# Kernel optimization log

Measured on AMD Instinct MI355X. Metric: run time of the kernel, lower is better.

Reference implementation:

```python
import jax, jax.numpy as jnp
import numpy as np

B, C, H, W = 2, 256, 64, 64  # C = in_channels; x has 2*C channels
DQ = C // 16


def setup_inputs() -> dict:
    key = jax.random.key(0)
    ks = jax.random.split(key, 10)
    s = 0.05
    return {
        "x": jax.random.normal(ks[0], (B, 2 * C, H, W), dtype=jnp.float32),
        "Wq": jax.random.normal(ks[1], (DQ, C), dtype=jnp.float32) * s,
        "bq": jax.random.normal(ks[2], (DQ,), dtype=jnp.float32) * s,
        "Wk": jax.random.normal(ks[3], (DQ, C), dtype=jnp.float32) * s,
        "bk": jax.random.normal(ks[4], (DQ,), dtype=jnp.float32) * s,
        "Wv": jax.random.normal(ks[5], (C, C), dtype=jnp.float32) * s,
        "bv": jax.random.normal(ks[6], (C,), dtype=jnp.float32) * s,
        "Wpt": jax.random.normal(ks[7], (C, 2 * C), dtype=jnp.float32) * s,
        "bpt": jax.random.normal(ks[8], (C,), dtype=jnp.float32) * s,
        "gamma": jnp.full((1,), 0.5, dtype=jnp.float32),  # original inits to 0; nonzero for a non-trivial output
    }


def _conv1x1(x, Wt, b):
    # 1x1 conv == per-pixel linear map over channels
    return jnp.einsum("bchw,dc->bdhw", x, Wt) + b[None, :, None, None]


def reference(x, Wq, bq, Wk, bk, Wv, bv, Wpt, bpt, gamma):
    n = x.shape[1] // 2
    x1, x2 = x[:, :n], x[:, n:]
    b, c, h, w = x1.shape
    hw = h * w

    def qkv(xi):
        q = _conv1x1(xi, Wq, bq).reshape(b, DQ, hw)   # [B,dq,HW]
        k = _conv1x1(xi, Wk, bk).reshape(b, DQ, hw)   # [B,dq,HW]
        v = _conv1x1(xi, Wv, bv).reshape(b, c, hw)    # [B,C,HW]
        return q, k, v

    q1, k1, v1 = qkv(x1)
    q2, k2, v2 = qkv(x2)

    # attn[b,i,j] = softmax_j( q[:,i] . k[:,j] )  (no scaling, as in original)
    attn1 = jax.nn.softmax(jnp.einsum("bdi,bdj->bij", q1, k1), axis=-1)  # [B,HW,HW]
    attn2 = jax.nn.softmax(jnp.einsum("bdi,bdj->bij", q2, k2), axis=-1)

    def apply_attn(v, attn):
        # out[b,c,i] = sum_j v[b,c,j] * attn[b,i,j]
        return jnp.einsum("bcj,bij->bci", v, attn).reshape(b, c, h, w)

    out11 = apply_attn(v1, attn1)
    out12 = apply_attn(v2, attn1)
    out21 = apply_attn(v1, attn2)
    out22 = apply_attn(v2, attn2)

    o1 = _conv1x1(jnp.concatenate([out11, out12], axis=1), Wpt, bpt)  # [B,C,H,W]
    o2 = _conv1x1(jnp.concatenate([out21, out22], axis=1), Wpt, bpt)

    out = gamma * jnp.concatenate([o1, o2], axis=1) + x
    return out
```

## Files before the change

kernel.cpp:

```cpp
#include <hip/hip_runtime.h>
#include <hip/hip_bf16.h>


#define HW 4096
#define CC 256
#define DQ 16

typedef __hip_bfloat16 bf16;
struct alignas(8) bh4 { bf16 x, y, z, w; };
typedef __bf16 bf16x8 __attribute__((ext_vector_type(8)));
typedef float  f32x4  __attribute__((ext_vector_type(4)));

static __device__ __forceinline__ float b2f(bf16 v) { return __bfloat162float(v); }
static __device__ __forceinline__ float ldf(const void* p, size_t i, bool isb) {
    return isb ? b2f(((const bf16*)p)[i]) : ((const float*)p)[i];
}

static __device__ __forceinline__ void load_lds16(const void* g, void* l) {
    __builtin_amdgcn_global_load_lds(
        (const __attribute__((address_space(1))) unsigned int*)g,
        (__attribute__((address_space(3))) unsigned int*)l, 16, 0, 0);
}

static __device__ __forceinline__ bf16x8 ones8() {
    union { unsigned int u[4]; bf16x8 v; } t;
    t.u[0] = t.u[1] = t.u[2] = t.u[3] = 0x3F803F80u;
    return t.v;
}

__global__ void __launch_bounds__(256)
prep_xt(const void* __restrict__ xsrc,
        const void* __restrict__ Wq_r, const void* __restrict__ bq_r,
        const void* __restrict__ Wk_r, const void* __restrict__ bk_r,
        const void* __restrict__ Wv_r, const void* __restrict__ bv_r,
        const void* __restrict__ Wpt_r, const void* __restrict__ bpt_r,
        const void* __restrict__ gam_r,
        float* __restrict__ bqf, float* __restrict__ bkf, float* __restrict__ gamf,
        bf16* __restrict__ Wqb, bf16* __restrict__ Wkb,
        bf16* __restrict__ McB, float* __restrict__ btot, bf16* __restrict__ Xt,
        const unsigned short* __restrict__ probe) {
    __shared__ float T[64][65];
    int bx = blockIdx.x, tid = threadIdx.x;
    bool isb = probe[0] != 0;
    if (bx < 512) {
        int d = bx >> 1;
        int c = ((bx & 1) << 8) + tid;
        int half = c >> 8, cm = c & 255;
        float acc = 0.f;
        for (int e = 0; e < 256; ++e)
            acc = fmaf(ldf(Wpt_r, (size_t)d * 512 + half * 256 + e, isb),
                       ldf(Wv_r, (size_t)e * 256 + cm, isb), acc);
        McB[d * 512 + c] = __float2bfloat16(acc);
    } else if (bx == 512) {
        int d = tid;
        float acc = ldf(bpt_r, d, isb);
        for (int e = 0; e < 256; ++e)
            acc = fmaf(ldf(Wpt_r, (size_t)d * 512 + e, isb) +
                       ldf(Wpt_r, (size_t)d * 512 + 256 + e, isb),
                       ldf(bv_r, e, isb), acc);
        btot[d] = acc;
    } else if (bx < 545) {
        int id = bx - 513;
        const void* s = id < 16 ? Wq_r : Wk_r;
        bf16* dst = id < 16 ? Wqb : Wkb;
        int i = (id & 15) * 256 + tid;
        dst[i] = __float2bfloat16(ldf(s, i, isb));
    } else if (bx == 545) {
        if (tid < 16) bqf[tid] = ldf(bq_r, tid, isb);
        else if (tid < 32) bkf[tid - 16] = ldf(bk_r, tid - 16, isb);
        else if (tid == 32) gamf[0] = ldf(gam_r, 0, isb);
    } else {
        int id = bx - 546;
        int j0 = (id & 63) * 64, e0 = ((id >> 6) & 7) * 64, b = id >> 9;
        int j_l = tid & 63, er0 = (tid >> 6) * 16;
#pragma unroll
        for (int r = 0; r < 16; ++r) {
            size_t src = ((size_t)(b * 512 + e0 + er0 + r)) * HW + j0 + j_l;
            T[er0 + r][j_l] = ldf(xsrc, src, isb);
        }
        __syncthreads();
        int e_w = tid & 63, jr0 = (tid >> 6) * 16;
#pragma unroll
        for (int r = 0; r < 16; ++r)
            Xt[((size_t)b * HW + j0 + jr0 + r) * 512 + e0 + e_w] =
                __float2bfloat16(T[e_w][jr0 + r]);
    }
}

__global__ void __launch_bounds__(256, 2)
qku(const bf16* __restrict__ Xt,
    const bf16* __restrict__ Wqb, const float* __restrict__ bqf,
    const bf16* __restrict__ Wkb, const float* __restrict__ bkf,
    bf16* __restrict__ Qb, bf16* __restrict__ Kb,
    const bf16* __restrict__ McB, bf16* __restrict__ Ub) {
    __shared__ __align__(16) bf16 sA[64 * 64];
    __shared__ __align__(16) bf16 sB[128 * 64];
    int tid = threadIdx.x;
    int lane = tid & 63, wave = tid >> 6;
    int ln = lane & 15, q = lane >> 4;
    int bx = blockIdx.x;

    if (bx < 256) {
        int bh = bx >> 6;
        int b = bh >> 1, h = bh & 1;
        int j0 = (bx & 63) * 64 + wave * 16;
        bf16x8 aQ[8], aK[8];
#pragma unroll
        for (int kk = 0; kk < 8; ++kk) {
            aQ[kk] = *(const bf16x8*)&Wqb[ln * 256 + kk * 32 + q * 8];
            aK[kk] = *(const bf16x8*)&Wkb[ln * 256 + kk * 32 + q * 8];
        }
        const bf16* Xrow = Xt + ((size_t)b * HW + j0 + ln) * 512 + h * 256;
        f32x4 dQ = {0.f, 0.f, 0.f, 0.f}, dK = {0.f, 0.f, 0.f, 0.f};
#pragma unroll
        for (int kk = 0; kk < 8; ++kk) {
            bf16x8 bxv = *(const bf16x8*)&Xrow[kk * 32 + q * 8];
            dQ = __builtin_amdgcn_mfma_f32_16x16x32_bf16(aQ[kk], bxv, dQ, 0, 0, 0);
            dK = __builtin_amdgcn_mfma_f32_16x16x32_bf16(aK[kk], bxv, dK, 0, 0, 0);
        }
        size_t rowoff = ((size_t)bh * HW + j0 + ln) * 32;
        bh4 oq, ok;
        oq.x = __float2bfloat16(dQ[0] + bqf[q * 4 + 0]);
        oq.y = __float2bfloat16(dQ[1] + bqf[q * 4 + 1]);
        oq.z = __float2bfloat16(dQ[2] + bqf[q * 4 + 2]);
        oq.w = __float2bfloat16(dQ[3] + bqf[q * 4 + 3]);
        ok.x = __float2bfloat16(dK[0] + bkf[q * 4 + 0]);
        ok.y = __float2bfloat16(dK[1] + bkf[q * 4 + 1]);
        ok.z = __float2bfloat16(dK[2] + bkf[q * 4 + 2]);
        ok.w = __float2bfloat16(dK[3] + bkf[q * 4 + 3]);
        bh4 z; z.x = z.y = z.z = z.w = __float2bfloat16(0.f);
        *(bh4*)&Qb[rowoff + q * 4] = oq;
        *(bh4*)&Qb[rowoff + 16 + q * 4] = z;
        *(bh4*)&Kb[rowoff + q * 4] = ok;
        *(bh4*)&Kb[rowoff + 16 + q * 4] = z;
        return;
    }

    int id = bx - 256;
    int wm = (wave >> 1) * 32, wn = (wave & 1) * 64;
    int j0 = (id & 31) * 128, c0 = ((id >> 5) & 3) * 64, b = id >> 7;
    const bf16* Xb = Xt + (size_t)b * HW * 512;
    f32x4 acc[2][4];
#pragma unroll
    for (int mi = 0; mi < 2; ++mi)
#pragma unroll
        for (int ni = 0; ni < 4; ++ni)
#pragma unroll
            for (int r = 0; r < 4; ++r) acc[mi][ni][r] = 0.f;

    for (int e0 = 0; e0 < 512; e0 += 64) {
        __syncthreads();
#pragma unroll
        for (int r = 0; r < 2; ++r) {
            int s = r * 256 + tid;
            int row = s >> 3, jc = s & 7, jg = jc ^ (row & 7);
            load_lds16(McB + (size_t)(c0 + row) * 512 + e0 + jg * 8, sA + s * 8);
        }
#pragma unroll
        for (int r = 0; r < 4; ++r) {
            int s = r * 256 + tid;
            int row = s >> 3, jc = s & 7, jg = jc ^ (row & 7);
            load_lds16(Xb + (size_t)(j0 + row) * 512 + e0 + jg * 8, sB + s * 8);
        }
        __syncthreads();
#pragma unroll
        for (int kh = 0; kh < 2; ++kh) {
            bf16x8 af[2], bfv[4];
#pragma unroll
            for (int mi = 0; mi < 2; ++mi) {
                int row = wm + mi * 16 + ln;
                int jc = (kh * 4 + q) ^ (row & 7);
                af[mi] = *(const bf16x8*)&sA[row * 64 + jc * 8];
            }
#pragma unroll
            for (int ni = 0; ni < 4; ++ni) {
                int row = wn + ni * 16 + ln;
                int jc = (kh * 4 + q) ^ (row & 7);
                bfv[ni] = *(const bf16x8*)&sB[row * 64 + jc * 8];
            }
#pragma unroll
            for (int mi = 0; mi < 2; ++mi)
#pragma unroll
                for (int ni = 0; ni < 4; ++ni)
                    acc[mi][ni] = __builtin_amdgcn_mfma_f32_16x16x32_bf16(
                        af[mi], bfv[ni], acc[mi][ni], 0, 0, 0);
        }
    }
#pragma unroll
    for (int mi = 0; mi < 2; ++mi)
#pragma unroll
        for (int r = 0; r < 4; ++r) {
            int c = c0 + wm + mi * 16 + q * 4 + r;
#pragma unroll
            for (int ni = 0; ni < 4; ++ni) {
                int j = j0 + wn + ni * 16 + ln;
                Ub[((size_t)(b * CC + c)) * HW + j] = __float2bfloat16(acc[mi][ni][r]);
            }
        }
}

__global__ void __launch_bounds__(256, 2)
flash_attn(const bf16* __restrict__ Ub, const bf16* __restrict__ Qb,
           const bf16* __restrict__ Kb, const float* __restrict__ btot,
           const void* __restrict__ xorig, const float* __restrict__ gamf,
           void* __restrict__ outv, const unsigned short* __restrict__ probe) {
    __shared__ __align__(16) bf16 sU[2][128 * 64];
    __shared__ __align__(16) bf16 sK[2][4 * 64 * 8];
    __shared__ __align__(16) bf16 sE[64 * 64];
    int tid  = threadIdx.x;
    int lane = tid & 63, wave = tid >> 6;
    int ln = lane & 15, q = lane >> 4;
    int wm = (wave & 1) * 64, wn = (wave >> 1) * 32;

    int bid = blockIdx.x;
    int panel = bid & 7;
    int i0 = (bid >> 3) * 64;
    int c0 = (panel & 1) * 128;
    int bh = panel >> 1;
    int b = bh >> 1, h = bh & 1;

    const bf16* Ubb = Ub + (size_t)b * CC * HW + (size_t)c0 * HW;
    const bf16* Kbh = Kb + (size_t)bh * HW * 32;
    const bf16x8 ONE = ones8();

    bf16x8 bq = *(const bf16x8*)&Qb[((size_t)bh * HW + i0 + wave * 16 + ln) * 32 + q * 8];

    f32x4 acc[4][2], accS[2];
#pragma unroll
    for (int ni = 0; ni < 2; ++ni) {
#pragma unroll
        for (int r = 0; r < 4; ++r) accS[ni][r] = 0.f;
#pragma unroll
        for (int mi = 0; mi < 4; ++mi)
#pragma unroll
            for (int r = 0; r < 4; ++r) acc[mi][ni][r] = 0.f;
    }

    int i_loc = wave * 16 + ln;
    int wchunk0 = (q >> 1);
    int woff = (q & 1) * 4;

    auto stage_u = [&](int tn, int bufn) {
#pragma unroll
        for (int r = 0; r < 4; ++r) {
            int s = r * 256 + tid;
            int row = s >> 3, jc = s & 7, jg = jc ^ (row & 7);
            load_lds16(Ubb + (size_t)row * HW + tn * 64 + jg * 8, &sU[bufn][s * 8]);
        }
    };
    auto stage_k = [&](int tn, int bufn) {
        load_lds16(Kbh + ((size_t)(tn * 64 + (tid >> 6) * 16 + (tid & 15))) * 32
                       + ((tid >> 4) & 3) * 8,
                   &sK[bufn][tid * 8]);
    };

    stage_u(0, 0);
    stage_k(0, 0);
    asm volatile("s_waitcnt vmcnt(0)" ::: "memory");
    __builtin_amdgcn_sched_barrier(0);
    __builtin_amdgcn_s_barrier();
    __builtin_amdgcn_sched_barrier(0);

    for (int t = 0; t < 64; ++t) {
        stage_u((t + 1) & 63, (t + 1) & 1);
        stage_k((t + 1) & 63, (t + 1) & 1);

        const bf16* sKc = sK[t & 1];
#pragma unroll
        for (int js = 0; js < 4; ++js) {
            bf16x8 ak = *(const bf16x8*)&sKc[(js * 64 + lane) * 8];
            f32x4 d = {0.f, 0.f, 0.f, 0.f};
            d = __builtin_amdgcn_mfma_f32_16x16x32_bf16(ak, bq, d, 0, 0, 0);
            bh4 o;
            o.x = __float2bfloat16(__expf(d[0]));
            o.y = __float2bfloat16(__expf(d[1]));
            o.z = __float2bfloat16(__expf(d[2]));
            o.w = __float2bfloat16(__expf(d[3]));
            int chunk = (js * 2 + wchunk0) ^ (i_loc & 7);
            *(bh4*)&sE[i_loc * 64 + chunk * 8 + woff] = o;
        }

        asm volatile("s_waitcnt lgkmcnt(0)" ::: "memory");
        __builtin_amdgcn_sched_barrier(0);
        __builtin_amdgcn_s_barrier();
        __builtin_amdgcn_sched_barrier(0);

        const bf16* sUc = sU[t & 1];
        __builtin_amdgcn_s_setprio(1);
#pragma unroll
        for (int kh = 0; kh < 2; ++kh) {
            bf16x8 af[4], bfv[2];
#pragma unroll
            for (int mi = 0; mi < 4; ++mi) {
                int row = wm + mi * 16 + ln;
                int jc = (kh * 4 + q) ^ (row & 7);
                af[mi] = *(const bf16x8*)&sUc[row * 64 + jc * 8];
            }
#pragma unroll
            for (int ni = 0; ni < 2; ++ni) {
                int row = wn + ni * 16 + ln;
                int jc = (kh * 4 + q) ^ (row & 7);
                bfv[ni] = *(const bf16x8*)&sE[row * 64 + jc * 8];
            }
#pragma unroll
            for (int ni = 0; ni < 2; ++ni) {
                accS[ni] = __builtin_amdgcn_mfma_f32_16x16x32_bf16(
                    ONE, bfv[ni], accS[ni], 0, 0, 0);
#pragma unroll
                for (int mi = 0; mi < 4; ++mi)
                    acc[mi][ni] = __builtin_amdgcn_mfma_f32_16x16x32_bf16(
                        af[mi], bfv[ni], acc[mi][ni], 0, 0, 0);
            }
        }
        __builtin_amdgcn_s_setprio(0);

        asm volatile("s_waitcnt vmcnt(0) lgkmcnt(0)" ::: "memory");
        __builtin_amdgcn_sched_barrier(0);
        __builtin_amdgcn_s_barrier();
        __builtin_amdgcn_sched_barrier(0);
    }

    bool isb = probe[0] != 0;
    float g = gamf[0];
    float lv[2];
#pragma unroll
    for (int ni = 0; ni < 2; ++ni)
        lv[ni] = 1.f / accS[ni][0];
#pragma unroll
    for (int mi = 0; mi < 4; ++mi)
#pragma unroll
        for (int r = 0; r < 4; ++r) {
            int c = c0 + wm + mi * 16 + q * 4 + r;
            float bt = btot[c];
            size_t rowbase = ((size_t)(b * 512 + h * 256 + c)) * HW + i0 + wn;
#pragma unroll
            for (int ni = 0; ni < 2; ++ni) {
                size_t idx = rowbase + ni * 16 + ln;
                float xres = isb ? b2f(((const bf16*)xorig)[idx]) : ((const float*)xorig)[idx];
                float o = fmaf(g, fmaf(acc[mi][ni][r], lv[ni], bt), xres);
                if (isb) ((bf16*)outv)[idx] = __float2bfloat16(o);
                else     ((float*)outv)[idx] = o;
            }
        }
}

extern "C" void kernel_launch(void* const* d_in, const int* in_sizes, int n_in,
                              void* d_out, int out_size, void* d_ws, size_t ws_size,
                              hipStream_t stream) {
    const unsigned short* probe = (const unsigned short*)d_in[9];

    char* ws = (char*)d_ws;
    size_t off = 0;
    auto alloc = [&](size_t bytes) { size_t r = off; off = (off + bytes + 255) & ~(size_t)255; return r; };
    float* bqf  = (float*)(ws + alloc(16 * 4));
    float* bkf  = (float*)(ws + alloc(16 * 4));
    float* gamf = (float*)(ws + alloc(4));
    bf16*  Xt   = (bf16*)(ws + alloc((size_t)2 * HW * 512 * 2));
    bf16*  McB  = (bf16*)(ws + alloc(256 * 512 * 2));
    float* btot = (float*)(ws + alloc(256 * 4));
    bf16*  Wqb  = (bf16*)(ws + alloc(DQ * 256 * 2));
    bf16*  Wkb  = (bf16*)(ws + alloc(DQ * 256 * 2));
    bf16*  Qb   = (bf16*)(ws + alloc((size_t)4 * HW * 32 * 2));
    bf16*  Kb   = (bf16*)(ws + alloc((size_t)4 * HW * 32 * 2));
    bf16*  Ub   = (bf16*)(ws + alloc((size_t)2 * CC * HW * 2));

    prep_xt<<<dim3(1570), 256, 0, stream>>>(
        d_in[0], d_in[1], d_in[2], d_in[3], d_in[4], d_in[5], d_in[6],
        d_in[7], d_in[8], d_in[9],
        bqf, bkf, gamf, Wqb, Wkb, McB, btot, Xt, probe);

    qku<<<dim3(512), 256, 0, stream>>>(Xt, Wqb, bqf, Wkb, bkf, Qb, Kb, McB, Ub);

    flash_attn<<<dim3(512), 256, 0, stream>>>(Ub, Qb, Kb, btot, d_in[0], gamf, d_out, probe);
}
```

Baseline: 245.8 us.

## Make each wave own its query rows in flash attention, drop mid-loop barrier

The flash-attention kernel now has each wave compute and consume its own 16 query rows of exp-scores through a per-wave LDS slice. This removes the block-wide barrier between the score and PV phases and the extra ones-matrix MFMA that computed row sums. Row sums are now accumulated in registers with shuffles. Each wave now reads all 128 U rows from LDS (8 A-fragments per B), which raises LDS read traffic per MFMA. The prep kernel's weight-fold loops also gain multiple accumulators and unrolling for ILP.

```diff
diff --git a/kernel.cpp b/kernel.cpp
--- a/kernel.cpp
+++ b/kernel.cpp
@@ -20,12 +20,6 @@
     __builtin_amdgcn_global_load_lds(
         (const __attribute__((address_space(1))) unsigned int*)g,
         (__attribute__((address_space(3))) unsigned int*)l, 16, 0, 0);
-}
-
-static __device__ __forceinline__ bf16x8 ones8() {
-    union { unsigned int u[4]; bf16x8 v; } t;
-    t.u[0] = t.u[1] = t.u[2] = t.u[3] = 0x3F803F80u;
-    return t.v;
 }
 
 __global__ void __launch_bounds__(256)
@@ -46,19 +40,46 @@
         int d = bx >> 1;
         int c = ((bx & 1) << 8) + tid;
         int half = c >> 8, cm = c & 255;
-        float acc = 0.f;
-        for (int e = 0; e < 256; ++e)
-            acc = fmaf(ldf(Wpt_r, (size_t)d * 512 + half * 256 + e, isb),
-                       ldf(Wv_r, (size_t)e * 256 + cm, isb), acc);
-        McB[d * 512 + c] = __float2bfloat16(acc);
+        size_t wp = (size_t)d * 512 + half * 256;
+        float a0 = 0.f, a1 = 0.f, a2 = 0.f, a3 = 0.f;
+        if (isb) {
+            const bf16* Wp = (const bf16*)Wpt_r + wp;
+            const bf16* Wv = (const bf16*)Wv_r + cm;
+#pragma unroll 8
+            for (int e = 0; e < 256; e += 4) {
+                a0 = fmaf(b2f(Wp[e + 0]), b2f(Wv[(size_t)(e + 0) * 256]), a0);
+                a1 = fmaf(b2f(Wp[e + 1]), b2f(Wv[(size_t)(e + 1) * 256]), a1);
+                a2 = fmaf(b2f(Wp[e + 2]), b2f(Wv[(size_t)(e + 2) * 256]), a2);
+                a3 = fmaf(b2f(Wp[e + 3]), b2f(Wv[(size_t)(e + 3) * 256]), a3);
+            }
+        } else {
+            const float* Wp = (const float*)Wpt_r + wp;
+            const float* Wv = (const float*)Wv_r + cm;
+#pragma unroll 8
+            for (int e = 0; e < 256; e += 4) {
+                a0 = fmaf(Wp[e + 0], Wv[(size_t)(e + 0) * 256], a0);
+                a1 = fmaf(Wp[e + 1], Wv[(size_t)(e + 1) * 256], a1);
+                a2 = fmaf(Wp[e + 2], Wv[(size_t)(e + 2) * 256], a2);
+                a3 = fmaf(Wp[e + 3], Wv[(size_t)(e + 3) * 256], a3);
+            }
+        }
+        McB[d * 512 + c] = __float2bfloat16((a0 + a1) + (a2 + a3));
     } else if (bx == 512) {
         int d = tid;
-        float acc = ldf(bpt_r, d, isb);
-        for (int e = 0; e < 256; ++e)
-            acc = fmaf(ldf(Wpt_r, (size_t)d * 512 + e, isb) +
-                       ldf(Wpt_r, (size_t)d * 512 + 256 + e, isb),
-                       ldf(bv_r, e, isb), acc);
-        btot[d] = acc;
+        float a0 = 0.f, a1 = 0.f, a2 = 0.f, a3 = 0.f;
+        float a4 = 0.f, a5 = 0.f, a6 = 0.f, a7 = 0.f;
+#pragma unroll 4
+        for (int e = 0; e < 256; e += 8) {
+            a0 = fmaf(ldf(Wpt_r, (size_t)d * 512 + e + 0, isb) + ldf(Wpt_r, (size_t)d * 512 + 256 + e + 0, isb), ldf(bv_r, e + 0, isb), a0);
+            a1 = fmaf(ldf(Wpt_r, (size_t)d * 512 + e + 1, isb) + ldf(Wpt_r, (size_t)d * 512 + 256 + e + 1, isb), ldf(bv_r, e + 1, isb), a1);
+            a2 = fmaf(ldf(Wpt_r, (size_t)d * 512 + e + 2, isb) + ldf(Wpt_r, (size_t)d * 512 + 256 + e + 2, isb), ldf(bv_r, e + 2, isb), a2);
+            a3 = fmaf(ldf(Wpt_r, (size_t)d * 512 + e + 3, isb) + ldf(Wpt_r, (size_t)d * 512 + 256 + e + 3, isb), ldf(bv_r, e + 3, isb), a3);
+            a4 = fmaf(ldf(Wpt_r, (size_t)d * 512 + e + 4, isb) + ldf(Wpt_r, (size_t)d * 512 + 256 + e + 4, isb), ldf(bv_r, e + 4, isb), a4);
+            a5 = fmaf(ldf(Wpt_r, (size_t)d * 512 + e + 5, isb) + ldf(Wpt_r, (size_t)d * 512 + 256 + e + 5, isb), ldf(bv_r, e + 5, isb), a5);
+            a6 = fmaf(ldf(Wpt_r, (size_t)d * 512 + e + 6, isb) + ldf(Wpt_r, (size_t)d * 512 + 256 + e + 6, isb), ldf(bv_r, e + 6, isb), a6);
+            a7 = fmaf(ldf(Wpt_r, (size_t)d * 512 + e + 7, isb) + ldf(Wpt_r, (size_t)d * 512 + 256 + e + 7, isb), ldf(bv_r, e + 7, isb), a7);
+        }
+        btot[d] = ldf(bpt_r, d, isb) + (((a0 + a1) + (a2 + a3)) + ((a4 + a5) + (a6 + a7)));
     } else if (bx < 545) {
         int id = bx - 513;
         const void* s = id < 16 ? Wq_r : Wk_r;
@@ -206,11 +227,10 @@
            void* __restrict__ outv, const unsigned short* __restrict__ probe) {
     __shared__ __align__(16) bf16 sU[2][128 * 64];
     __shared__ __align__(16) bf16 sK[2][4 * 64 * 8];
-    __shared__ __align__(16) bf16 sE[64 * 64];
+    __shared__ __align__(16) bf16 sE[4][16 * 64];
     int tid  = threadIdx.x;
     int lane = tid & 63, wave = tid >> 6;
     int ln = lane & 15, q = lane >> 4;
-    int wm = (wave & 1) * 64, wn = (wave >> 1) * 32;
 
     int bid = blockIdx.x;
     int panel = bid & 7;
@@ -221,24 +241,16 @@
 
     const bf16* Ubb = Ub + (size_t)b * CC * HW + (size_t)c0 * HW;
     const bf16* Kbh = Kb + (size_t)bh * HW * 32;
-    const bf16x8 ONE = ones8();
+    bf16* sEw = &sE[wave][0];
 
     bf16x8 bq = *(const bf16x8*)&Qb[((size_t)bh * HW + i0 + wave * 16 + ln) * 32 + q * 8];
 
-    f32x4 acc[4][2], accS[2];
-#pragma unroll
-    for (int ni = 0; ni < 2; ++ni) {
-#pragma unroll
-        for (int r = 0; r < 4; ++r) accS[ni][r] = 0.f;
-#pragma unroll
-        for (int mi = 0; mi < 4; ++mi)
-#pragma unroll
-            for (int r = 0; r < 4; ++r) acc[mi][ni][r] = 0.f;
-    }
-
-    int i_loc = wave * 16 + ln;
-    int wchunk0 = (q >> 1);
-    int woff = (q & 1) * 4;
+    f32x4 acc[8];
+#pragma unroll
+    for (int mi = 0; mi < 8; ++mi)
+#pragma unroll
+        for (int r = 0; r < 4; ++r) acc[mi][r] = 0.f;
+    float lsum = 0.f;
 
     auto stage_u = [&](int tn, int bufn) {
 #pragma unroll
@@ -271,45 +283,33 @@
             bf16x8 ak = *(const bf16x8*)&sKc[(js * 64 + lane) * 8];
             f32x4 d = {0.f, 0.f, 0.f, 0.f};
             d = __builtin_amdgcn_mfma_f32_16x16x32_bf16(ak, bq, d, 0, 0, 0);
+            float e0 = __expf(d[0]), e1 = __expf(d[1]);
+            float e2 = __expf(d[2]), e3 = __expf(d[3]);
+            lsum += (e0 + e1) + (e2 + e3);
             bh4 o;
-            o.x = __float2bfloat16(__expf(d[0]));
-            o.y = __float2bfloat16(__expf(d[1]));
-            o.z = __float2bfloat16(__expf(d[2]));
-            o.w = __float2bfloat16(__expf(d[3]));
-            int chunk = (js * 2 + wchunk0) ^ (i_loc & 7);
-            *(bh4*)&sE[i_loc * 64 + chunk * 8 + woff] = o;
+            o.x = __float2bfloat16(e0);
+            o.y = __float2bfloat16(e1);
+            o.z = __float2bfloat16(e2);
+            o.w = __float2bfloat16(e3);
+            int chunk = (js * 2 + (q >> 1)) ^ (ln & 7);
+            *(bh4*)&sEw[ln * 64 + chunk * 8 + (q & 1) * 4] = o;
         }
 
         asm volatile("s_waitcnt lgkmcnt(0)" ::: "memory");
         __builtin_amdgcn_sched_barrier(0);
-        __builtin_amdgcn_s_barrier();
-        __builtin_amdgcn_sched_barrier(0);
 
         const bf16* sUc = sU[t & 1];
         __builtin_amdgcn_s_setprio(1);
 #pragma unroll
         for (int kh = 0; kh < 2; ++kh) {
-            bf16x8 af[4], bfv[2];
-#pragma unroll
-            for (int mi = 0; mi < 4; ++mi) {
-                int row = wm + mi * 16 + ln;
+            bf16x8 bfv = *(const bf16x8*)&sEw[ln * 64 + (((kh * 4 + q) ^ (ln & 7)) * 8)];
+#pragma unroll
+            for (int mi = 0; mi < 8; ++mi) {
+                int row = mi * 16 + ln;
                 int jc = (kh * 4 + q) ^ (row & 7);
-                af[mi] = *(const bf16x8*)&sUc[row * 64 + jc * 8];
-            }
-#pragma unroll
-            for (int ni = 0; ni < 2; ++ni) {
-                int row = wn + ni * 16 + ln;
-                int jc = (kh * 4 + q) ^ (row & 7);
-                bfv[ni] = *(const bf16x8*)&sE[row * 64 + jc * 8];
-            }
-#pragma unroll
-            for (int ni = 0; ni < 2; ++ni) {
-                accS[ni] = __builtin_amdgcn_mfma_f32_16x16x32_bf16(
-                    ONE, bfv[ni], accS[ni], 0, 0, 0);
-#pragma unroll
-                for (int mi = 0; mi < 4; ++mi)
-                    acc[mi][ni] = __builtin_amdgcn_mfma_f32_16x16x32_bf16(
-                        af[mi], bfv[ni], acc[mi][ni], 0, 0, 0);
+                bf16x8 af = *(const bf16x8*)&sUc[row * 64 + jc * 8];
+                acc[mi] = __builtin_amdgcn_mfma_f32_16x16x32_bf16(
+                    af, bfv, acc[mi], 0, 0, 0);
             }
         }
         __builtin_amdgcn_s_setprio(0);
@@ -320,27 +320,23 @@
         __builtin_amdgcn_sched_barrier(0);
     }
 
+    lsum += __shfl_xor(lsum, 16);
+    lsum += __shfl_xor(lsum, 32);
+    float lv = 1.f / lsum;
+
     bool isb = probe[0] != 0;
     float g = gamf[0];
-    float lv[2];
-#pragma unroll
-    for (int ni = 0; ni < 2; ++ni)
-        lv[ni] = 1.f / accS[ni][0];
-#pragma unroll
-    for (int mi = 0; mi < 4; ++mi)
+#pragma unroll
+    for (int mi = 0; mi < 8; ++mi)
 #pragma unroll
         for (int r = 0; r < 4; ++r) {
-            int c = c0 + wm + mi * 16 + q * 4 + r;
+            int c = c0 + mi * 16 + q * 4 + r;
             float bt = btot[c];
-            size_t rowbase = ((size_t)(b * 512 + h * 256 + c)) * HW + i0 + wn;
-#pragma unroll
-            for (int ni = 0; ni < 2; ++ni) {
-                size_t idx = rowbase + ni * 16 + ln;
-                float xres = isb ? b2f(((const bf16*)xorig)[idx]) : ((const float*)xorig)[idx];
-                float o = fmaf(g, fmaf(acc[mi][ni][r], lv[ni], bt), xres);
-                if (isb) ((bf16*)outv)[idx] = __float2bfloat16(o);
-                else     ((float*)outv)[idx] = o;
-            }
+            size_t idx = ((size_t)(b * 512 + h * 256 + c)) * HW + i0 + wave * 16 + ln;
+            float xres = isb ? b2f(((const bf16*)xorig)[idx]) : ((const float*)xorig)[idx];
+            float o = fmaf(g, fmaf(acc[mi][r], lv, bt), xres);
+            if (isb) ((bf16*)outv)[idx] = __float2bfloat16(o);
+            else     ((float*)outv)[idx] = o;
         }
 }
 
```

Measured after the change: 259.8 us. 1.06x slower.
